# Performance work log

Measured on AMD Instinct MI355X. Metric: run time of the kernel, lower is better.

The kernel has to match this reference:

```python
import jax, jax.numpy as jnp
import numpy as np

N, D, NUM_CLASSES = 8192, 64, 16
EPS = 1e-7


def setup_inputs() -> dict:
    key = jax.random.key(0)
    k1, k2 = jax.random.split(key)
    raw = jax.random.normal(k1, (N, D), dtype=jnp.float32)
    # project into the open Poincare ball: norm < 0.9
    nrm = jnp.linalg.norm(raw, axis=-1, keepdims=True)
    points = raw * (0.9 / (1.0 + nrm))
    labels = jax.random.randint(k2, (N,), 0, NUM_CLASSES, dtype=jnp.int64)
    return {"points": points, "labels": labels}


def _poincare_dist_matrix(x):
    # d(x,y) = arccosh(1 + 2||x-y||^2 / ((1-||x||^2)(1-||y||^2)))
    sq = jnp.sum(x * x, axis=-1)                      # [N]
    sqdist = jnp.maximum(sq[:, None] + sq[None, :] - 2.0 * (x @ x.T), 0.0)  # [N,N]
    denom = jnp.maximum((1.0 - sq)[:, None] * (1.0 - sq)[None, :], EPS)
    arg = jnp.maximum(1.0 + 2.0 * sqdist / denom, 1.0 + EPS)
    return jnp.arccosh(arg)


def reference(points, labels):
    d = _poincare_dist_matrix(points)                 # [N,N]
    logits = -d
    n = logits.shape[0]
    diag = jnp.eye(n, dtype=bool)
    neg_inf = jnp.finfo(logits.dtype).min
    # log A_i = logsumexp_{a != i} (-d_ia)
    logA = jax.nn.logsumexp(jnp.where(diag, neg_inf, logits), axis=1)  # [N]
    pos = (labels[:, None] == labels[None, :]) & (~diag)               # [N,N]
    P = jnp.sum(pos, axis=1).astype(logits.dtype)                      # [N]
    p_sum = jnp.sum(jnp.where(pos, logits - logA[:, None], 0.0), axis=1)
    return jnp.sum(-p_sum / P)
```

## Files before the change

kernel.cpp:

```cpp
#include <hip/hip_runtime.h>

#define NPTS 8192
#define DIM 64
#define EPSF 1e-7f
#define LN2F 0.69314718055994531f
#define NBLK 1056
#define PERSIST 768

typedef unsigned short u16;
typedef __attribute__((ext_vector_type(8))) short bf16x8;
typedef __attribute__((ext_vector_type(8))) unsigned short u16x8;
typedef __attribute__((ext_vector_type(4))) float f32x4;

__global__ void prep_kernel(const float* __restrict__ x, const int* __restrict__ labels,
                            u16* __restrict__ hi,
                            float4* __restrict__ meta,
                            float* __restrict__ S, float* __restrict__ T,
                            float* __restrict__ out) {
    int g = blockIdx.x * blockDim.x + threadIdx.x;
    int row = g >> 3, sub = g & 7;
    const float* xp = x + row * DIM + sub * 8;
    float v[8];
    float s = 0.f;
#pragma unroll
    for (int k = 0; k < 8; k++) { v[k] = xp[k]; s = fmaf(v[k], v[k], s); }
    s += __shfl_xor(s, 1);
    s += __shfl_xor(s, 2);
    s += __shfl_xor(s, 4);
    u16x8 h;
#pragma unroll
    for (int k = 0; k < 8; k++) {
        unsigned int bits = __float_as_uint(v[k]);
        unsigned int r = bits + 0x7FFFu + ((bits >> 16) & 1u);
        h[k] = (u16)(r >> 16);
    }
    *(u16x8*)(hi + row * DIM + sub * 8) = h;
    if (sub == 0) {
        float r = 1.0f / (1.0f - s);
        meta[row] = make_float4(-0.5f * s, r, -4.0f * r, (float)labels[row]);
    } else if (sub == 1) {
        S[row] = 0.f;
    } else if (sub == 2) {
        T[row] = 0.f;
    }
    if (g == 3) out[0] = 0.f;
}

__device__ __forceinline__ int cumtiles(int b) { return 65 * b - b * b; }

__global__ void __launch_bounds__(256, 3) pair_mfma(
        const u16* __restrict__ hi,
        const float4* __restrict__ meta,
        float* __restrict__ Sarr, float* __restrict__ Tarr) {
    __shared__ float slabS[4][256], slabT[4][256];

    int tid = threadIdx.x;
    int wave = tid >> 6, lane = tid & 63;
    int quad = lane >> 4, l15 = lane & 15;

#pragma unroll 1
    for (int widx = 0; widx < 2; widx++) {
        int bid = blockIdx.x + widx * PERSIST;
        if (bid >= NBLK) break;

        int by = (int)((65.0f - __builtin_amdgcn_sqrtf(4225.0f - 4.0f * (float)bid)) * 0.5f);
        while (cumtiles(by + 1) <= bid) by++;
        while (cumtiles(by) > bid) by--;
        int off = bid - cumtiles(by);
        int bx = 2 * by + off;
        bool full = (off >= 2);

        int i0 = bx * 128 + wave * 32;
        int j0 = by * 256;

        bf16x8 a_hi[2][2];
#pragma unroll
        for (int it = 0; it < 2; it++)
#pragma unroll
            for (int ks = 0; ks < 2; ks++) {
                int aoff = (i0 + it * 16 + l15) * DIM + ks * 32 + quad * 8;
                a_hi[it][ks] = *(const bf16x8*)(hi + aoff);
            }

        float hsqi[8], rcpi[8], labi[8];
#pragma unroll
        for (int it = 0; it < 2; it++)
#pragma unroll
            for (int r = 0; r < 4; r++) {
                float4 m = meta[i0 + it * 16 + quad * 4 + r];
                hsqi[it * 4 + r] = m.x;
                rcpi[it * 4 + r] = m.y;
                labi[it * 4 + r] = m.w;
            }

        if (full) {
            slabS[wave][lane] = 0.f;       slabT[wave][lane] = 0.f;
            slabS[wave][lane + 64] = 0.f;  slabT[wave][lane + 64] = 0.f;
            slabS[wave][lane + 128] = 0.f; slabT[wave][lane + 128] = 0.f;
            slabS[wave][lane + 192] = 0.f; slabT[wave][lane + 192] = 0.f;
        }

        float Sx[8], Tx[8];
#pragma unroll
        for (int k = 0; k < 8; k++) { Sx[k] = 0.f; Tx[k] = 0.f; }

#pragma unroll 4
        for (int t = 0; t < 16; t++) {
            int jg = j0 + t * 16 + l15;
            bf16x8 b_hi[2];
            int boff = jg * DIM + quad * 8;
            b_hi[0] = *(const bf16x8*)(hi + boff);
            b_hi[1] = *(const bf16x8*)(hi + boff + 32);
            float4 mj = meta[jg];

            float pS = 0.f, pT = 0.f;
#pragma unroll
            for (int it = 0; it < 2; it++) {
                f32x4 acc0, acc1;
#pragma unroll
                for (int r = 0; r < 4; r++) { acc0[r] = hsqi[it * 4 + r] + mj.x; acc1[r] = 0.f; }
                acc0 = __builtin_amdgcn_mfma_f32_16x16x32_bf16(a_hi[it][0], b_hi[0], acc0, 0, 0, 0);
                acc1 = __builtin_amdgcn_mfma_f32_16x16x32_bf16(a_hi[it][1], b_hi[1], acc1, 0, 0, 0);

#pragma unroll
                for (int r = 0; r < 4; r++) {
                    int idx = it * 4 + r;
                    float D = acc0[r] + acc1[r];
                    float u = fmaxf(D * rcpi[idx] * mj.z, EPSF);
                    float srt = __builtin_amdgcn_sqrtf(fmaf(u, u, u + u));
                    float opu = 1.0f + u;
                    float st = opu - srt;
                    float l2 = __builtin_amdgcn_logf(opu + srt);
                    float tv = (mj.w == labi[idx]) ? l2 : 0.0f;
                    Sx[idx] += st;
                    Tx[idx] += tv;
                    pS += st; pT += tv;
                }
            }

            if (full) {
                pS += __shfl_xor(pS, 16); pS += __shfl_xor(pS, 32);
                pT += __shfl_xor(pT, 16); pT += __shfl_xor(pT, 32);
                if (quad == 0) {
                    int c = t * 16 + l15;
                    slabS[wave][c] += pS;
                    slabT[wave][c] += pT;
                }
            }
        }

#pragma unroll
        for (int r = 0; r < 8; r++) {
#pragma unroll
            for (int m = 1; m < 16; m <<= 1) {
                Sx[r] += __shfl_xor(Sx[r], m);
                Tx[r] += __shfl_xor(Tx[r], m);
            }
        }
        if (l15 == 0) {
#pragma unroll
            for (int it = 0; it < 2; it++)
#pragma unroll
                for (int r = 0; r < 4; r++) {
                    int row = i0 + it * 16 + quad * 4 + r;
                    atomicAdd(&Sarr[row], Sx[it * 4 + r]);
                    atomicAdd(&Tarr[row], Tx[it * 4 + r]);
                }
        }

        if (full) {
            __syncthreads();
            float s = slabS[0][tid] + slabS[1][tid] + slabS[2][tid] + slabS[3][tid];
            float tt = slabT[0][tid] + slabT[1][tid] + slabT[2][tid] + slabT[3][tid];
            atomicAdd(&Sarr[j0 + tid], s);
            atomicAdd(&Tarr[j0 + tid], tt);
        }
        if (widx == 0 && blockIdx.x + PERSIST < NBLK)
            __syncthreads();
    }
}

__global__ void __launch_bounds__(256) finalize_kernel(
        const float* __restrict__ S, const float* __restrict__ T,
        const int* __restrict__ labels, float* __restrict__ out) {
    __shared__ int hist[16][16];
    __shared__ float cntf[16];
    __shared__ float red[256];
    int tid = threadIdx.x;
    hist[tid >> 4][tid & 15] = 0;
    __syncthreads();
    int rep = tid & 15;
    for (int i = tid; i < NPTS; i += 256)
        atomicAdd(&hist[rep][labels[i]], 1);
    __syncthreads();
    if (tid < 16) {
        int s = 0;
#pragma unroll
        for (int k = 0; k < 16; k++) s += hist[k][tid];
        cntf[tid] = (float)(s - 1);
    }
    __syncthreads();

    float s0 = __builtin_amdgcn_sqrtf(EPSF * (2.0f + EPSF));
    float st0 = 1.0f + EPSF - s0;
    float l20 = __builtin_amdgcn_logf(1.0f + EPSF + s0);
    int i = blockIdx.x * 256 + tid;
    float loss = __logf(S[i] - st0) + (T[i] - l20) * LN2F / cntf[labels[i]];
    red[tid] = loss;
    __syncthreads();
    for (int s = 128; s > 0; s >>= 1) {
        if (tid < s) red[tid] += red[tid + s];
        __syncthreads();
    }
    if (tid == 0) atomicAdd(out, red[0]);
}

extern "C" void kernel_launch(void* const* d_in, const int* in_sizes, int n_in,
                              void* d_out, int out_size, void* d_ws, size_t ws_size,
                              hipStream_t stream) {
    const float* x = (const float*)d_in[0];
    const int* labels = (const int*)d_in[1];

    u16* hi = (u16*)d_ws;
    float4* meta = (float4*)(hi + NPTS * DIM);
    float* S = (float*)(meta + NPTS);
    float* T = S + NPTS;

    prep_kernel<<<(NPTS * 8) / 256, 256, 0, stream>>>(x, labels, hi, meta, S, T, (float*)d_out);

    pair_mfma<<<PERSIST, 256, 0, stream>>>(hi, meta, S, T);

    finalize_kernel<<<NPTS / 256, 256, 0, stream>>>(S, T, labels, (float*)d_out);
}
```

Measured before the change: 104.9 us.

## Drop persistent loop, vectorize epilogue math, replace LDS column slab with per-wave atomics

After: 237.8 us. 2.27x slower.

```diff
diff --git a/kernel.cpp b/kernel.cpp
--- a/kernel.cpp
+++ b/kernel.cpp
@@ -5,12 +5,12 @@
 #define EPSF 1e-7f
 #define LN2F 0.69314718055994531f
 #define NBLK 1056
-#define PERSIST 768
 
 typedef unsigned short u16;
 typedef __attribute__((ext_vector_type(8))) short bf16x8;
 typedef __attribute__((ext_vector_type(8))) unsigned short u16x8;
 typedef __attribute__((ext_vector_type(4))) float f32x4;
+typedef __attribute__((ext_vector_type(2))) float f32x2;
 
 __global__ void prep_kernel(const float* __restrict__ x, const int* __restrict__ labels,
                             u16* __restrict__ hi,
@@ -52,131 +52,125 @@
         const u16* __restrict__ hi,
         const float4* __restrict__ meta,
         float* __restrict__ Sarr, float* __restrict__ Tarr) {
-    __shared__ float slabS[4][256], slabT[4][256];
-
     int tid = threadIdx.x;
     int wave = tid >> 6, lane = tid & 63;
     int quad = lane >> 4, l15 = lane & 15;
 
-#pragma unroll 1
-    for (int widx = 0; widx < 2; widx++) {
-        int bid = blockIdx.x + widx * PERSIST;
-        if (bid >= NBLK) break;
-
-        int by = (int)((65.0f - __builtin_amdgcn_sqrtf(4225.0f - 4.0f * (float)bid)) * 0.5f);
-        while (cumtiles(by + 1) <= bid) by++;
-        while (cumtiles(by) > bid) by--;
-        int off = bid - cumtiles(by);
-        int bx = 2 * by + off;
-        bool full = (off >= 2);
-
-        int i0 = bx * 128 + wave * 32;
-        int j0 = by * 256;
-
-        bf16x8 a_hi[2][2];
+    int bid = blockIdx.x;
+    int by = (int)((65.0f - __builtin_amdgcn_sqrtf(4225.0f - 4.0f * (float)bid)) * 0.5f);
+    while (cumtiles(by + 1) <= bid) by++;
+    while (cumtiles(by) > bid) by--;
+    int off = bid - cumtiles(by);
+    int bx = 2 * by + off;
+    bool full = (off >= 2);
+
+    int i0 = bx * 128 + wave * 32;
+    int j0 = by * 256;
+
+    bf16x8 a_hi[2][2];
+#pragma unroll
+    for (int it = 0; it < 2; it++)
+#pragma unroll
+        for (int ks = 0; ks < 2; ks++) {
+            int aoff = (i0 + it * 16 + l15) * DIM + ks * 32 + quad * 8;
+            a_hi[it][ks] = *(const bf16x8*)(hi + aoff);
+        }
+
+    f32x4 hsqi4[2];
+    f32x2 rcp2[4];
+    float labi[8];
+#pragma unroll
+    for (int it = 0; it < 2; it++)
+#pragma unroll
+        for (int r = 0; r < 4; r++) {
+            float4 m = meta[i0 + it * 16 + quad * 4 + r];
+            hsqi4[it][r] = m.x;
+            rcp2[it * 2 + (r >> 1)][r & 1] = m.y;
+            labi[it * 4 + r] = m.w;
+        }
+
+    f32x2 Sx2[4], Tx2[4];
+#pragma unroll
+    for (int k = 0; k < 4; k++) { Sx2[k] = (f32x2){0.f, 0.f}; Tx2[k] = (f32x2){0.f, 0.f}; }
+
+    float psS[16], psT[16];
+
+#pragma unroll
+    for (int t = 0; t < 16; t++) {
+        int jg = j0 + t * 16 + l15;
+        int boff = jg * DIM + quad * 8;
+        bf16x8 b0 = *(const bf16x8*)(hi + boff);
+        bf16x8 b1 = *(const bf16x8*)(hi + boff + 32);
+        float4 mj = meta[jg];
+
+        f32x2 sSum = (f32x2){0.f, 0.f}, tSum = (f32x2){0.f, 0.f};
+#pragma unroll
+        for (int it = 0; it < 2; it++) {
+            f32x4 acc = hsqi4[it] + mj.x;
+            acc = __builtin_amdgcn_mfma_f32_16x16x32_bf16(a_hi[it][0], b0, acc, 0, 0, 0);
+            acc = __builtin_amdgcn_mfma_f32_16x16x32_bf16(a_hi[it][1], b1, acc, 0, 0, 0);
+
+#pragma unroll
+            for (int g = 0; g < 2; g++) {
+                f32x2 D = (f32x2){acc[2 * g], acc[2 * g + 1]};
+                f32x2 u = (D * rcp2[it * 2 + g]) * mj.z;
+                u = __builtin_elementwise_max(u, (f32x2){EPSF, EPSF});
+                f32x2 arg = u * u + (u + u);
+                f32x2 srt = (f32x2){__builtin_amdgcn_sqrtf(arg.x), __builtin_amdgcn_sqrtf(arg.y)};
+                f32x2 opu = u + 1.0f;
+                f32x2 st = opu - srt;
+                f32x2 w1 = opu + srt;
+                f32x2 l2 = (f32x2){__builtin_amdgcn_logf(w1.x), __builtin_amdgcn_logf(w1.y)};
+                f32x2 tv;
+                tv.x = (mj.w == labi[it * 4 + 2 * g]) ? l2.x : 0.0f;
+                tv.y = (mj.w == labi[it * 4 + 2 * g + 1]) ? l2.y : 0.0f;
+                Sx2[it * 2 + g] += st;
+                Tx2[it * 2 + g] += tv;
+                sSum += st;
+                tSum += tv;
+            }
+        }
+        psS[t] = sSum.x + sSum.y;
+        psT[t] = tSum.x + tSum.y;
+    }
+
+    float Sx[8], Tx[8];
+#pragma unroll
+    for (int k = 0; k < 4; k++) {
+        Sx[2 * k] = Sx2[k].x; Sx[2 * k + 1] = Sx2[k].y;
+        Tx[2 * k] = Tx2[k].x; Tx[2 * k + 1] = Tx2[k].y;
+    }
+#pragma unroll
+    for (int r = 0; r < 8; r++) {
+#pragma unroll
+        for (int m = 1; m < 16; m <<= 1) {
+            Sx[r] += __shfl_xor(Sx[r], m);
+            Tx[r] += __shfl_xor(Tx[r], m);
+        }
+    }
+    if (l15 == 0) {
 #pragma unroll
         for (int it = 0; it < 2; it++)
 #pragma unroll
-            for (int ks = 0; ks < 2; ks++) {
-                int aoff = (i0 + it * 16 + l15) * DIM + ks * 32 + quad * 8;
-                a_hi[it][ks] = *(const bf16x8*)(hi + aoff);
+            for (int r = 0; r < 4; r++) {
+                int row = i0 + it * 16 + quad * 4 + r;
+                atomicAdd(&Sarr[row], Sx[it * 4 + r]);
+                atomicAdd(&Tarr[row], Tx[it * 4 + r]);
             }
-
-        float hsqi[8], rcpi[8], labi[8];
-#pragma unroll
-        for (int it = 0; it < 2; it++)
-#pragma unroll
-            for (int r = 0; r < 4; r++) {
-                float4 m = meta[i0 + it * 16 + quad * 4 + r];
-                hsqi[it * 4 + r] = m.x;
-                rcpi[it * 4 + r] = m.y;
-                labi[it * 4 + r] = m.w;
+    }
+
+    if (full) {
+#pragma unroll
+        for (int t = 0; t < 16; t++) {
+            float s = psS[t], tt = psT[t];
+            s += __shfl_xor(s, 16); s += __shfl_xor(s, 32);
+            tt += __shfl_xor(tt, 16); tt += __shfl_xor(tt, 32);
+            if (quad == 0) {
+                int col = j0 + t * 16 + l15;
+                atomicAdd(&Sarr[col], s);
+                atomicAdd(&Tarr[col], tt);
             }
-
-        if (full) {
-            slabS[wave][lane] = 0.f;       slabT[wave][lane] = 0.f;
-            slabS[wave][lane + 64] = 0.f;  slabT[wave][lane + 64] = 0.f;
-            slabS[wave][lane + 128] = 0.f; slabT[wave][lane + 128] = 0.f;
-            slabS[wave][lane + 192] = 0.f; slabT[wave][lane + 192] = 0.f;
-        }
-
-        float Sx[8], Tx[8];
-#pragma unroll
-        for (int k = 0; k < 8; k++) { Sx[k] = 0.f; Tx[k] = 0.f; }
-
-#pragma unroll 4
-        for (int t = 0; t < 16; t++) {
-            int jg = j0 + t * 16 + l15;
-            bf16x8 b_hi[2];
-            int boff = jg * DIM + quad * 8;
-            b_hi[0] = *(const bf16x8*)(hi + boff);
-            b_hi[1] = *(const bf16x8*)(hi + boff + 32);
-            float4 mj = meta[jg];
-
-            float pS = 0.f, pT = 0.f;
-#pragma unroll
-            for (int it = 0; it < 2; it++) {
-                f32x4 acc0, acc1;
-#pragma unroll
-                for (int r = 0; r < 4; r++) { acc0[r] = hsqi[it * 4 + r] + mj.x; acc1[r] = 0.f; }
-                acc0 = __builtin_amdgcn_mfma_f32_16x16x32_bf16(a_hi[it][0], b_hi[0], acc0, 0, 0, 0);
-                acc1 = __builtin_amdgcn_mfma_f32_16x16x32_bf16(a_hi[it][1], b_hi[1], acc1, 0, 0, 0);
-
-#pragma unroll
-                for (int r = 0; r < 4; r++) {
-                    int idx = it * 4 + r;
-                    float D = acc0[r] + acc1[r];
-                    float u = fmaxf(D * rcpi[idx] * mj.z, EPSF);
-                    float srt = __builtin_amdgcn_sqrtf(fmaf(u, u, u + u));
-                    float opu = 1.0f + u;
-                    float st = opu - srt;
-                    float l2 = __builtin_amdgcn_logf(opu + srt);
-                    float tv = (mj.w == labi[idx]) ? l2 : 0.0f;
-                    Sx[idx] += st;
-                    Tx[idx] += tv;
-                    pS += st; pT += tv;
-                }
-            }
-
-            if (full) {
-                pS += __shfl_xor(pS, 16); pS += __shfl_xor(pS, 32);
-                pT += __shfl_xor(pT, 16); pT += __shfl_xor(pT, 32);
-                if (quad == 0) {
-                    int c = t * 16 + l15;
-                    slabS[wave][c] += pS;
-                    slabT[wave][c] += pT;
-                }
-            }
-        }
-
-#pragma unroll
-        for (int r = 0; r < 8; r++) {
-#pragma unroll
-            for (int m = 1; m < 16; m <<= 1) {
-                Sx[r] += __shfl_xor(Sx[r], m);
-                Tx[r] += __shfl_xor(Tx[r], m);
-            }
-        }
-        if (l15 == 0) {
-#pragma unroll
-            for (int it = 0; it < 2; it++)
-#pragma unroll
-                for (int r = 0; r < 4; r++) {
-                    int row = i0 + it * 16 + quad * 4 + r;
-                    atomicAdd(&Sarr[row], Sx[it * 4 + r]);
-                    atomicAdd(&Tarr[row], Tx[it * 4 + r]);
-                }
-        }
-
-        if (full) {
-            __syncthreads();
-            float s = slabS[0][tid] + slabS[1][tid] + slabS[2][tid] + slabS[3][tid];
-            float tt = slabT[0][tid] + slabT[1][tid] + slabT[2][tid] + slabT[3][tid];
-            atomicAdd(&Sarr[j0 + tid], s);
-            atomicAdd(&Tarr[j0 + tid], tt);
-        }
-        if (widx == 0 && blockIdx.x + PERSIST < NBLK)
-            __syncthreads();
+        }
     }
 }
 
@@ -228,7 +222,7 @@
 
     prep_kernel<<<(NPTS * 8) / 256, 256, 0, stream>>>(x, labels, hi, meta, S, T, (float*)d_out);
 
-    pair_mfma<<<PERSIST, 256, 0, stream>>>(hi, meta, S, T);
+    pair_mfma<<<NBLK, 256, 0, stream>>>(hi, meta, S, T);
 
     finalize_kernel<<<NPTS / 256, 256, 0, stream>>>(S, T, labels, (float*)d_out);
 }
```
